# Performance work log

Measured on AMD Instinct MI355X. Metric: run time of the kernel, lower is better.

## Reference

```python
import jax, jax.numpy as jnp
import numpy as np

B, N, M, C = 4, 4096, 4096, 256
IMG_W, IMG_H = 1280.0, 384.0


def setup_inputs() -> dict:
    key = jax.random.key(0)
    ks = jax.random.split(key, 12)
    nodes_L = jax.random.normal(ks[0], (B, N, C), dtype=jnp.float32)
    nodes_R = jax.random.normal(ks[1], (B, M, C), dtype=jnp.float32)
    # pixel coordinates: (u, v) with u in [0, IMG_W), v in [0, IMG_H)
    scale = jnp.array([IMG_W, IMG_H], dtype=jnp.float32)
    kpts_L = jax.random.uniform(ks[2], (B, N, 2), dtype=jnp.float32) * scale
    kpts_R = jax.random.uniform(ks[3], (B, M, 2), dtype=jnp.float32) * scale
    s = 1.0 / np.sqrt(C)
    Wq = jax.random.normal(ks[4], (C, C), dtype=jnp.float32) * s
    bq = jnp.zeros((C,), dtype=jnp.float32)
    Wk = jax.random.normal(ks[5], (C, C), dtype=jnp.float32) * s
    bk = jnp.zeros((C,), dtype=jnp.float32)
    Wv = jax.random.normal(ks[6], (C, C), dtype=jnp.float32) * s
    bv = jnp.zeros((C,), dtype=jnp.float32)
    Wm = jax.random.normal(ks[7], (C, C), dtype=jnp.float32) * s
    bm = jnp.zeros((C,), dtype=jnp.float32)
    return {"nodes_L": nodes_L, "nodes_R": nodes_R, "kpts_L": kpts_L, "kpts_R": kpts_R,
            "Wq": Wq, "bq": bq, "Wk": Wk, "bk": bk, "Wv": Wv, "bv": bv, "Wm": Wm, "bm": bm}


def reference(nodes_L, nodes_R, kpts_L, kpts_R, Wq, bq, Wk, bk, Wv, bv, Wm, bm):
    dim = nodes_L.shape[-1]
    # torch Linear: x @ W.T + b
    Q = nodes_L @ Wq.T + bq                      # [B,N,C]
    K = nodes_R @ Wk.T + bk                      # [B,M,C]
    V = nodes_R @ Wv.T + bv                      # [B,M,C]
    # epipolar geometry terms, [B,N,M]
    dist_v = jnp.abs(kpts_L[:, :, 1:2] - kpts_R[:, :, 1][:, None, :])
    dist_u = kpts_L[:, :, 0:1] - kpts_R[:, :, 0][:, None, :]
    mask = (dist_v < 3.0) & (dist_u > 0) & (dist_u < 192)
    attn = jnp.einsum('bnc,bmc->bnm', Q, K) / jnp.sqrt(jnp.float32(dim))
    attn = jnp.where(mask, attn, jnp.float32(-1e9))
    attn_weights = jax.nn.softmax(attn, axis=-1)  # [B,N,M]
    matched = jnp.einsum('bnm,bmc->bnc', attn_weights, V)
    init_disparity = jnp.sum(attn_weights * dist_u, axis=-1, keepdims=True)  # [B,N,1]
    confidence = jnp.any(mask, axis=-1, keepdims=True).astype(jnp.float32)   # [B,N,1]
    return matched @ Wm.T + bm, init_disparity, confidence
```

## Files before the change

### kernel.cpp

```cpp
#include <hip/hip_runtime.h>
#include <hip/hip_bf16.h>

#define BB 4
#define NN 4096
#define MM 4096
#define CC 256
#define CAP 128
#define NBIN 384
#define NCH 16
#define CHK 256

typedef __attribute__((ext_vector_type(8))) short bf16x8;
typedef __attribute__((ext_vector_type(4))) float f32x4;

static __device__ __forceinline__ float bf2f(unsigned short u) {
    return __uint_as_float(((unsigned)u) << 16);
}
static __device__ __forceinline__ unsigned short f2bf(float f) {
    unsigned u = __float_as_uint(f);
    u += 0x7fffu + ((u >> 16) & 1u);
    return (unsigned short)(u >> 16);
}
static __device__ __forceinline__ bf16x8 asbf(uint4 u) {
    union { uint4 a; bf16x8 b; } c; c.a = u; return c.b;
}
static __device__ __forceinline__ void gload16(const unsigned short* g, unsigned short* l) {
    __builtin_amdgcn_global_load_lds(
        (const __attribute__((address_space(1))) unsigned int*)g,
        (__attribute__((address_space(3))) unsigned int*)l, 16, 0, 0);
}

__global__ __launch_bounds__(256) void prep_kernel(
    const float* __restrict__ Wq, const float* __restrict__ Wk,
    const float* __restrict__ Wv, const float* __restrict__ Wm,
    const float* __restrict__ L, const float* __restrict__ R,
    const float* __restrict__ kptsR,
    unsigned short* __restrict__ Wpk, unsigned short* __restrict__ Lpk,
    unsigned short* __restrict__ Rpk,
    int* __restrict__ hist, unsigned short* __restrict__ prank,
    float* __restrict__ Vsum, float* __restrict__ Usum)
{
    __shared__ __align__(16) unsigned char SMEM[32768];
    const int tid = threadIdx.x, y = blockIdx.y, x = blockIdx.x;

    if (y < 4) {
        const float* S = (y == 0) ? Wq : (y == 1) ? Wk : (y == 2) ? Wv : Wm;
        int o = x * 256 + tid;
        int j = o & 7, lane = (o >> 3) & 63, kt = o >> 9;
        int kk = kt >> 4, t = kt & 15;
        int r = t * 16 + (lane & 15), c = kk * 32 + (lane >> 4) * 8 + j;
        Wpk[(size_t)y * 65536 + o] = f2bf(S[r * 256 + c]);
        return;
    }
    if (y < 6) {
        const float* S = (y == 5) ? R : L;
        unsigned short* D = (y == 5) ? Rpk : Lpk;
        unsigned short* T = (unsigned short*)SMEM;
        const int wid = tid >> 6, lane = tid & 63;
        const size_t R0 = (size_t)x * 64;
#pragma unroll
        for (int it = 0; it < 16; ++it) {
            int row = it * 4 + wid;
            float4 f = *(const float4*)(S + (R0 + row) * 256 + lane * 4);
            ushort4 h = make_ushort4(f2bf(f.x), f2bf(f.y), f2bf(f.z), f2bf(f.w));
            int col = lane * 4;
            *(ushort4*)&T[row * 256 + (col ^ ((row & 7) << 3))] = h;
        }
        __syncthreads();
        unsigned short* Dp = D + (size_t)x * 16384;
#pragma unroll
        for (int p = 0; p < 8; ++p) {
            int u = p * 2048 + tid * 8;
            int rt = u >> 12, rem = u & 4095;
            int kk = rem >> 9, ln = (rem >> 3) & 63;
            int row = rt * 16 + (ln & 15);
            int col = kk * 32 + (ln >> 4) * 8;
            *(uint4*)(Dp + u) = *(const uint4*)&T[row * 256 + (col ^ ((row & 7) << 3))];
        }
        return;
    }
    if (y == 6) {
        if (x >= NCH * BB) return;
        int chunk = x & 15, b = x >> 4;
        int* h = (int*)SMEM;
        short* sbin = (short*)(SMEM + NBIN * 4);
        for (int i = tid; i < NBIN; i += CHK) h[i] = 0;
        int m = chunk * CHK + tid;
        float2 p = ((const float2*)kptsR)[(size_t)b * MM + m];
        int bin = (int)p.y;
        sbin[tid] = (short)bin;
        __syncthreads();
        atomicAdd(&h[bin], 1);
        int r = 0;
        for (int t = 0; t < tid; ++t) r += (sbin[t] == bin);
        prank[(b << 12) + m] = (unsigned short)r;
        __syncthreads();
        for (int i = tid; i < NBIN; i += CHK)
            hist[((size_t)b * NCH + chunk) * NBIN + i] = h[i];
        return;
    }
    if (x < BB) {
        int b = x;
        float s = 0.f;
        for (int m = tid; m < MM; m += 256) s += kptsR[((size_t)b * MM + m) * 2 + 0];
#pragma unroll
        for (int off = 32; off; off >>= 1) s += __shfl_xor(s, off);
        float* sr = (float*)SMEM;
        int wave = tid >> 6, lane = tid & 63;
        if (lane == 0) sr[wave] = s;
        __syncthreads();
        if (tid == 0) Usum[b] = sr[0] + sr[1] + sr[2] + sr[3];
    } else if (x == BB) {
        for (int i = tid; i < BB * CC; i += 256) Vsum[i] = 0.f;
    }
}

template <bool OUT_BF16>
__global__ __launch_bounds__(256, 4) void proj_mfma_kernel(
    const unsigned short* __restrict__ A0, const unsigned short* __restrict__ A1,
    const unsigned short* __restrict__ A2, const unsigned short* __restrict__ Wpk,
    const float* __restrict__ b0, const float* __restrict__ b1, const float* __restrict__ b2,
    void* __restrict__ O0, void* __restrict__ O1, void* __restrict__ O2,
    float* __restrict__ Vsum,
    const int* __restrict__ hist, int* __restrict__ binStart,
    const float* __restrict__ kptsR, const unsigned short* __restrict__ prank,
    unsigned short* __restrict__ sortedM, float2* __restrict__ sortedUV)
{
    __shared__ __align__(16) unsigned char SMEM[32768];
    const int tid = threadIdx.x, wid = tid >> 6, lane = tid & 63;
    const int y = blockIdx.y;

    if (y == 3) {
        if (blockIdx.x >= NCH * BB) return;
        const int b = blockIdx.x >> 4, chunk = blockIdx.x & 15;
        int* h2 = (int*)SMEM;
        int* sc = (int*)(SMEM + 24576);
        for (int i = tid; i < NCH * NBIN; i += 256)
            h2[i] = hist[(size_t)b * NCH * NBIN + i];
        __syncthreads();
        for (int v = tid; v < NBIN; v += 256) {
            int tot = 0;
#pragma unroll
            for (int c = 0; c < NCH; ++c) tot += h2[c * NBIN + v];
            sc[v] = tot;
        }
        __syncthreads();
        for (int off = 1; off < NBIN; off <<= 1) {
            int v1 = tid + 256;
            int t0 = (tid >= off) ? sc[tid - off] : 0;
            int t1 = (v1 < NBIN && v1 >= off) ? sc[v1 - off] : 0;
            __syncthreads();
            sc[tid] += t0;
            if (v1 < NBIN) sc[v1] += t1;
            __syncthreads();
        }
        if (chunk == 0) {
            for (int v = tid; v < NBIN; v += 256)
                binStart[b * (NBIN + 1) + v] = v ? sc[v - 1] : 0;
            if (tid == 0) binStart[b * (NBIN + 1) + NBIN] = sc[NBIN - 1];
        }
        int m = chunk * CHK + tid;
        float2 p = ((const float2*)kptsR)[(size_t)b * MM + m];
        int bin = (int)p.y;
        int ex = bin ? sc[bin - 1] : 0;
        for (int c = 0; c < chunk; ++c) ex += h2[c * NBIN + bin];
        int pos = ex + prank[(b << 12) + m];
        sortedM[(b << 12) + pos] = (unsigned short)m;
        sortedUV[(b << 12) + pos] = p;
        return;
    }

    const int lrow = lane & 15, lk = lane >> 4;
    const unsigned short* A = (y == 0) ? A0 : (y == 1) ? A1 : A2;
    const float* bias = (y == 0) ? b0 : (y == 1) ? b1 : b2;
    void* Out = (y == 0) ? O0 : (y == 1) ? O1 : O2;
    const unsigned short* W = Wpk + (size_t)y * 65536;

    const int bid = blockIdx.x;
    const int g = (bid >> 3) & 3;
    const int rblk = (bid & 7) + ((bid >> 5) << 3);
    const size_t rbase = (size_t)rblk * 128;
    const int rt0 = rblk * 8 + wid * 2;

    unsigned short* Wl = (unsigned short*)SMEM;
#pragma unroll
    for (int i = 0; i < 8; ++i) {
        int kk = wid * 2 + (i >> 2), q = i & 3;
        gload16(W + (size_t)kk * 8192 + g * 2048 + q * 512 + lane * 8,
                Wl + kk * 2048 + q * 512 + lane * 8);
    }

    const unsigned short* Ap = A + (size_t)rt0 * 4096 + lane * 8;
    uint4 a[2][2];
    a[0][0] = *(const uint4*)(Ap);
    a[0][1] = *(const uint4*)(Ap + 4096);

    f32x4 acc[4][2];
#pragma unroll
    for (int t = 0; t < 4; ++t) {
        acc[t][0] = (f32x4){0.f, 0.f, 0.f, 0.f};
        acc[t][1] = (f32x4){0.f, 0.f, 0.f, 0.f};
    }

    asm volatile("s_waitcnt vmcnt(0)" ::: "memory");
    __syncthreads();

#pragma unroll
    for (int kk = 0; kk < 8; ++kk) {
        const int cur = kk & 1, nxt = cur ^ 1;
        if (kk < 7) {
            a[nxt][0] = *(const uint4*)(Ap + (kk + 1) * 512);
            a[nxt][1] = *(const uint4*)(Ap + 4096 + (kk + 1) * 512);
        }
        bf16x8 af0 = asbf(a[cur][0]);
        bf16x8 af1 = asbf(a[cur][1]);
#pragma unroll
        for (int t = 0; t < 4; ++t) {
            bf16x8 wf = *(const bf16x8*)(Wl + kk * 2048 + t * 512 + lane * 8);
            acc[t][0] = __builtin_amdgcn_mfma_f32_16x16x32_bf16(af0, wf, acc[t][0], 0, 0, 0);
            acc[t][1] = __builtin_amdgcn_mfma_f32_16x16x32_bf16(af1, wf, acc[t][1], 0, 0, 0);
        }
    }

    if (Vsum != nullptr && y == 2) {
#pragma unroll
        for (int t = 0; t < 4; ++t) {
            int col = g * 64 + t * 16 + lrow;
            float vs = acc[t][0][0] + acc[t][0][1] + acc[t][0][2] + acc[t][0][3]
                     + acc[t][1][0] + acc[t][1][1] + acc[t][1][2] + acc[t][1][3];
            vs += __shfl_xor(vs, 16);
            vs += __shfl_xor(vs, 32);
            if (lk == 0)
                atomicAdd(&Vsum[(rblk >> 5) * CC + col], vs + 32.f * bias[col]);
        }
    }

    __syncthreads();
    if constexpr (OUT_BF16) {
        unsigned short* Bo = (unsigned short*)SMEM;
#pragma unroll
        for (int t = 0; t < 4; ++t) {
            float bb = bias[g * 64 + t * 16 + lrow];
#pragma unroll
            for (int s = 0; s < 2; ++s)
#pragma unroll
                for (int rr = 0; rr < 4; ++rr) {
                    int row = wid * 32 + s * 16 + lk * 4 + rr;
                    Bo[row * 64 + t * 16 + lrow] = f2bf(acc[t][s][rr] + bb);
                }
        }
        __syncthreads();
        unsigned short* O = (unsigned short*)Out;
#pragma unroll
        for (int it = 0; it < 4; ++it) {
            int idx = it * 2048 + tid * 8;
            int row = idx >> 6, col = idx & 63;
            *(uint4*)(O + (rbase + row) * CC + g * 64 + col) = *(const uint4*)&Bo[idx];
        }
    } else {
        float* Bo = (float*)SMEM;
#pragma unroll
        for (int t = 0; t < 4; ++t) {
            float bb = bias[g * 64 + t * 16 + lrow];
#pragma unroll
            for (int s = 0; s < 2; ++s)
#pragma unroll
                for (int rr = 0; rr < 4; ++rr) {
                    int row = wid * 32 + s * 16 + lk * 4 + rr;
                    Bo[row * 64 + t * 16 + lrow] = acc[t][s][rr] + bb;
                }
        }
        __syncthreads();
        float* O = (float*)Out;
#pragma unroll
        for (int it = 0; it < 8; ++it) {
            int idx = it * 1024 + tid * 4;
            int row = idx >> 6, col = idx & 63;
            *(float4*)(O + (rbase + row) * CC + g * 64 + col) = *(const float4*)&Bo[idx];
        }
    }
}

static __device__ __forceinline__ size_t mt_po(int bn, int lane) {
    return ((size_t)(bn >> 4)) * 4096 + (size_t)(lane >> 3) * 512
         + (size_t)(((lane >> 1) & 3) * 16 + (bn & 15)) * 8 + (lane & 1) * 4;
}

__global__ __launch_bounds__(256) void attn_kernel(
    const unsigned short* __restrict__ Q, const unsigned short* __restrict__ K,
    const unsigned short* __restrict__ V,
    const float* __restrict__ kptsL,
    const int* __restrict__ binStart, const unsigned short* __restrict__ sortedM,
    const float2* __restrict__ sortedUV,
    const float* __restrict__ Vsum, const float* __restrict__ Usum,
    unsigned short* __restrict__ Mpk, float* __restrict__ out1, float* __restrict__ out2)
{
    __shared__ unsigned short s_m[4][CAP];
    __shared__ float s_du[4][CAP];
    __shared__ float s_p[4][CAP];

    const int wid = threadIdx.x >> 6, lane = threadIdx.x & 63;
    const int bn = blockIdx.x * 4 + wid;
    const int b = bn >> 12;

    const int gi = lane >> 4, c = lane & 15;
    float qf[16];
    {
        const unsigned short* Qr = Q + (size_t)bn * CC + c * 16;
#pragma unroll
        for (int j = 0; j < 4; ++j) {
            ushort4 t = *(const ushort4*)(Qr + j * 4);
            qf[j * 4 + 0] = bf2f(t.x); qf[j * 4 + 1] = bf2f(t.y);
            qf[j * 4 + 2] = bf2f(t.z); qf[j * 4 + 3] = bf2f(t.w);
        }
    }

    float2 kl = *(const float2*)(kptsL + (size_t)bn * 2);
    float uL = kl.x, vL = kl.y;

    int ifl = (int)vL;
    int v0 = max(0, ifl - 3), v1 = min(NBIN - 1, ifl + 3);
    int s = binStart[b * (NBIN + 1) + v0];
    int e = binStart[b * (NBIN + 1) + v1 + 1];

    int cnt = 0;
    for (int i0 = s; i0 < e; i0 += 64) {
        int i = i0 + lane;
        bool valid = false;
        float du = 0.f;
        int m = 0;
        if (i < e) {
            float2 uv = sortedUV[(b << 12) + i];
            m = sortedM[(b << 12) + i];
            du = uL - uv.x;
            float dv = fabsf(vL - uv.y);
            valid = (dv < 3.0f) && (du > 0.0f) && (du < 192.0f);
        }
        unsigned long long bal = __ballot(valid);
        int pos = cnt + __popcll(bal & ((1ull << lane) - 1ull));
        if (valid && pos < CAP) { s_m[wid][pos] = (unsigned short)m; s_du[wid][pos] = du; }
        cnt += __popcll(bal);
    }
    if (cnt > CAP) cnt = CAP;

    if (cnt == 0) {
        float4 vs = *(const float4*)(Vsum + b * CC + lane * 4);
        ushort4 o = make_ushort4(f2bf(vs.x * (1.f / MM)), f2bf(vs.y * (1.f / MM)),
                                 f2bf(vs.z * (1.f / MM)), f2bf(vs.w * (1.f / MM)));
        *(ushort4*)(Mpk + mt_po(bn, lane)) = o;
        if (lane == 0) { out1[bn] = uL - Usum[b] * (1.f / MM); out2[bn] = 0.f; }
        return;
    }

    const unsigned short* Kb = K + (((size_t)b) << 12) * CC;
    for (int i0 = 0; i0 < cnt; i0 += 4) {
        int i = i0 + gi;
        int m = s_m[wid][(i < cnt) ? i : 0];
        const unsigned short* Kr = Kb + (size_t)m * CC + c * 16;
        float d = 0.f;
#pragma unroll
        for (int j = 0; j < 4; ++j) {
            ushort4 t = *(const ushort4*)(Kr + j * 4);
            d += qf[j * 4 + 0] * bf2f(t.x) + qf[j * 4 + 1] * bf2f(t.y)
               + qf[j * 4 + 2] * bf2f(t.z) + qf[j * 4 + 3] * bf2f(t.w);
        }
        d += __shfl_xor(d, 8); d += __shfl_xor(d, 4);
        d += __shfl_xor(d, 2); d += __shfl_xor(d, 1);
        if (c == 0 && i < cnt) s_p[wid][i] = d;
    }

    const float NEG = -3.0e38f;
    float mx, ps, ds, inv;
    if (cnt <= 64) {
        float x0 = (lane < cnt) ? s_p[wid][lane] * 0.0625f : NEG;
        mx = x0;
#pragma unroll
        for (int off = 32; off; off >>= 1) mx = fmaxf(mx, __shfl_xor(mx, off));
        float p0 = (lane < cnt) ? __expf(x0 - mx) : 0.f;
        float d0 = (lane < cnt) ? s_du[wid][lane] : 0.f;
        ps = p0; ds = p0 * d0;
#pragma unroll
        for (int off = 32; off; off >>= 1) { ps += __shfl_xor(ps, off); ds += __shfl_xor(ds, off); }
        inv = 1.f / ps;
        if (lane < cnt) s_p[wid][lane] = p0 * inv;
    } else {
        float x0 = (lane < cnt) ? s_p[wid][lane] * 0.0625f : NEG;
        float x1 = (lane + 64 < cnt) ? s_p[wid][lane + 64] * 0.0625f : NEG;
        mx = fmaxf(x0, x1);
#pragma unroll
        for (int off = 32; off; off >>= 1) mx = fmaxf(mx, __shfl_xor(mx, off));
        float p0 = (lane < cnt) ? __expf(x0 - mx) : 0.f;
        float p1 = (lane + 64 < cnt) ? __expf(x1 - mx) : 0.f;
        float d0 = (lane < cnt) ? s_du[wid][lane] : 0.f;
        float d1 = (lane + 64 < cnt) ? s_du[wid][lane + 64] : 0.f;
        ps = p0 + p1; ds = p0 * d0 + p1 * d1;
#pragma unroll
        for (int off = 32; off; off >>= 1) { ps += __shfl_xor(ps, off); ds += __shfl_xor(ds, off); }
        inv = 1.f / ps;
        if (lane < cnt) s_p[wid][lane] = p0 * inv;
        if (lane + 64 < cnt) s_p[wid][lane + 64] = p1 * inv;
    }

    const unsigned short* Vb = V + (((size_t)b) << 12) * CC;
    float a0 = 0.f, a1 = 0.f, a2 = 0.f, a3 = 0.f;
    float e0 = 0.f, e1 = 0.f, e2 = 0.f, e3 = 0.f;
    int i = 0;
    for (; i + 1 < cnt; i += 2) {
        float w0 = s_p[wid][i], w1 = s_p[wid][i + 1];
        ushort4 va = *(const ushort4*)(Vb + (size_t)s_m[wid][i] * CC + lane * 4);
        ushort4 vb = *(const ushort4*)(Vb + (size_t)s_m[wid][i + 1] * CC + lane * 4);
        a0 += w0 * bf2f(va.x); a1 += w0 * bf2f(va.y);
        a2 += w0 * bf2f(va.z); a3 += w0 * bf2f(va.w);
        e0 += w1 * bf2f(vb.x); e1 += w1 * bf2f(vb.y);
        e2 += w1 * bf2f(vb.z); e3 += w1 * bf2f(vb.w);
    }
    if (i < cnt) {
        float w0 = s_p[wid][i];
        ushort4 va = *(const ushort4*)(Vb + (size_t)s_m[wid][i] * CC + lane * 4);
        a0 += w0 * bf2f(va.x); a1 += w0 * bf2f(va.y);
        a2 += w0 * bf2f(va.z); a3 += w0 * bf2f(va.w);
    }
    ushort4 o = make_ushort4(f2bf(a0 + e0), f2bf(a1 + e1), f2bf(a2 + e2), f2bf(a3 + e3));
    *(ushort4*)(Mpk + mt_po(bn, lane)) = o;
    if (lane == 0) { out1[bn] = ds * inv; out2[bn] = 1.f; }
}

extern "C" void kernel_launch(void* const* d_in, const int* in_sizes, int n_in,
                              void* d_out, int out_size, void* d_ws, size_t ws_size,
                              hipStream_t stream) {
    const float* nodes_L = (const float*)d_in[0];
    const float* nodes_R = (const float*)d_in[1];
    const float* kpts_L  = (const float*)d_in[2];
    const float* kpts_R  = (const float*)d_in[3];
    const float* Wq = (const float*)d_in[4];
    const float* bq = (const float*)d_in[5];
    const float* Wk = (const float*)d_in[6];
    const float* bk = (const float*)d_in[7];
    const float* Wv = (const float*)d_in[8];
    const float* bv = (const float*)d_in[9];
    const float* Wm = (const float*)d_in[10];
    const float* bm = (const float*)d_in[11];

    char* ws = (char*)d_ws;
    unsigned short* Wpk = (unsigned short*)ws; ws += (size_t)4 * 65536 * 2;
    unsigned short* Lpk = (unsigned short*)ws; ws += (size_t)BB * NN * CC * 2;
    unsigned short* Rpk = (unsigned short*)ws; ws += (size_t)BB * MM * CC * 2;
    unsigned short* Qp  = (unsigned short*)ws; ws += (size_t)BB * NN * CC * 2;
    unsigned short* Kp  = (unsigned short*)ws; ws += (size_t)BB * MM * CC * 2;
    unsigned short* Vp  = (unsigned short*)ws; ws += (size_t)BB * MM * CC * 2;
    unsigned short* Mpk = (unsigned short*)ws; ws += (size_t)BB * NN * CC * 2;
    float* Vsum = (float*)ws;        ws += (size_t)BB * CC * 4;
    float* Usum = (float*)ws;        ws += (size_t)BB * 4;
    float2* sortedUV = (float2*)ws;  ws += (size_t)BB * MM * 8;
    int* binStart = (int*)ws;        ws += (size_t)BB * (NBIN + 1) * 4;
    unsigned short* sortedM = (unsigned short*)ws; ws += (size_t)BB * MM * 2;
    int* hist = (int*)ws;            ws += (size_t)BB * NCH * NBIN * 4;
    unsigned short* prank = (unsigned short*)ws;

    float* out0 = (float*)d_out;
    float* out1 = out0 + (size_t)BB * NN * CC;
    float* out2 = out1 + (size_t)BB * NN;

    prep_kernel<<<dim3(256, 8), dim3(256), 0, stream>>>(
        Wq, Wk, Wv, Wm, nodes_L, nodes_R, kpts_R,
        Wpk, Lpk, Rpk, hist, prank, Vsum, Usum);

    proj_mfma_kernel<true><<<dim3(512, 4), dim3(256), 0, stream>>>(
        Lpk, Rpk, Rpk, Wpk, bq, bk, bv, Qp, Kp, Vp, Vsum,
        hist, binStart, kpts_R, prank, sortedM, sortedUV);

    attn_kernel<<<dim3(BB * NN / 4), dim3(256), 0, stream>>>(
        Qp, Kp, Vp, kpts_L, binStart, sortedM, sortedUV, Vsum, Usum, Mpk, out1, out2);

    proj_mfma_kernel<false><<<dim3(512, 1), dim3(256), 0, stream>>>(
        Mpk, nullptr, nullptr, Wpk + 3 * 65536, bm, nullptr, nullptr,
        out0, nullptr, nullptr, nullptr,
        nullptr, nullptr, nullptr, nullptr, nullptr, nullptr);
}
```

Before: 62.77 us.

## Process left keypoints in v-bin sorted order for K/V locality in attention

```diff
diff --git a/kernel.cpp b/kernel.cpp
--- a/kernel.cpp
+++ b/kernel.cpp
@@ -34,10 +34,11 @@
     const float* __restrict__ Wq, const float* __restrict__ Wk,
     const float* __restrict__ Wv, const float* __restrict__ Wm,
     const float* __restrict__ L, const float* __restrict__ R,
-    const float* __restrict__ kptsR,
+    const float* __restrict__ kptsR, const float* __restrict__ kptsL,
     unsigned short* __restrict__ Wpk, unsigned short* __restrict__ Lpk,
     unsigned short* __restrict__ Rpk,
     int* __restrict__ hist, unsigned short* __restrict__ prank,
+    int* __restrict__ histL, unsigned short* __restrict__ prankL,
     float* __restrict__ Vsum, float* __restrict__ Usum)
 {
     __shared__ __align__(16) unsigned char SMEM[32768];
@@ -79,24 +80,27 @@
         }
         return;
     }
-    if (y == 6) {
+    if (y == 6 || y == 8) {
         if (x >= NCH * BB) return;
+        const float* KP = (y == 8) ? kptsL : kptsR;
+        int* H = (y == 8) ? histL : hist;
+        unsigned short* PR = (y == 8) ? prankL : prank;
         int chunk = x & 15, b = x >> 4;
         int* h = (int*)SMEM;
         short* sbin = (short*)(SMEM + NBIN * 4);
         for (int i = tid; i < NBIN; i += CHK) h[i] = 0;
         int m = chunk * CHK + tid;
-        float2 p = ((const float2*)kptsR)[(size_t)b * MM + m];
+        float2 p = ((const float2*)KP)[(size_t)b * MM + m];
         int bin = (int)p.y;
         sbin[tid] = (short)bin;
         __syncthreads();
         atomicAdd(&h[bin], 1);
         int r = 0;
         for (int t = 0; t < tid; ++t) r += (sbin[t] == bin);
-        prank[(b << 12) + m] = (unsigned short)r;
+        PR[(b << 12) + m] = (unsigned short)r;
         __syncthreads();
         for (int i = tid; i < NBIN; i += CHK)
-            hist[((size_t)b * NCH + chunk) * NBIN + i] = h[i];
+            H[((size_t)b * NCH + chunk) * NBIN + i] = h[i];
         return;
     }
     if (x < BB) {
@@ -122,21 +126,27 @@
     const float* __restrict__ b0, const float* __restrict__ b1, const float* __restrict__ b2,
     void* __restrict__ O0, void* __restrict__ O1, void* __restrict__ O2,
     float* __restrict__ Vsum,
-    const int* __restrict__ hist, int* __restrict__ binStart,
-    const float* __restrict__ kptsR, const unsigned short* __restrict__ prank,
-    unsigned short* __restrict__ sortedM, float2* __restrict__ sortedUV)
+    const int* __restrict__ hist, const int* __restrict__ histL,
+    int* __restrict__ binStart,
+    const float* __restrict__ kptsR, const float* __restrict__ kptsL,
+    const unsigned short* __restrict__ prank, const unsigned short* __restrict__ prankL,
+    unsigned short* __restrict__ sortedM, float2* __restrict__ sortedUV,
+    unsigned short* __restrict__ sortedNL)
 {
     __shared__ __align__(16) unsigned char SMEM[32768];
     const int tid = threadIdx.x, wid = tid >> 6, lane = tid & 63;
     const int y = blockIdx.y;
 
     if (y == 3) {
-        if (blockIdx.x >= NCH * BB) return;
-        const int b = blockIdx.x >> 4, chunk = blockIdx.x & 15;
+        if (blockIdx.x >= 2 * NCH * BB) return;
+        const int isL = blockIdx.x >= NCH * BB;
+        const int xx = blockIdx.x & (NCH * BB - 1);
+        const int b = xx >> 4, chunk = xx & 15;
+        const int* H = isL ? histL : hist;
         int* h2 = (int*)SMEM;
         int* sc = (int*)(SMEM + 24576);
         for (int i = tid; i < NCH * NBIN; i += 256)
-            h2[i] = hist[(size_t)b * NCH * NBIN + i];
+            h2[i] = H[(size_t)b * NCH * NBIN + i];
         __syncthreads();
         for (int v = tid; v < NBIN; v += 256) {
             int tot = 0;
@@ -154,19 +164,23 @@
             if (v1 < NBIN) sc[v1] += t1;
             __syncthreads();
         }
-        if (chunk == 0) {
+        if (!isL && chunk == 0) {
             for (int v = tid; v < NBIN; v += 256)
                 binStart[b * (NBIN + 1) + v] = v ? sc[v - 1] : 0;
             if (tid == 0) binStart[b * (NBIN + 1) + NBIN] = sc[NBIN - 1];
         }
         int m = chunk * CHK + tid;
-        float2 p = ((const float2*)kptsR)[(size_t)b * MM + m];
+        float2 p = ((const float2*)(isL ? kptsL : kptsR))[(size_t)b * MM + m];
         int bin = (int)p.y;
         int ex = bin ? sc[bin - 1] : 0;
         for (int c = 0; c < chunk; ++c) ex += h2[c * NBIN + bin];
-        int pos = ex + prank[(b << 12) + m];
-        sortedM[(b << 12) + pos] = (unsigned short)m;
-        sortedUV[(b << 12) + pos] = p;
+        int pos = ex + (isL ? prankL : prank)[(b << 12) + m];
+        if (isL) {
+            sortedNL[(b << 12) + pos] = (unsigned short)m;
+        } else {
+            sortedM[(b << 12) + pos] = (unsigned short)m;
+            sortedUV[(b << 12) + pos] = p;
+        }
         return;
     }
 
@@ -289,7 +303,7 @@
 __global__ __launch_bounds__(256) void attn_kernel(
     const unsigned short* __restrict__ Q, const unsigned short* __restrict__ K,
     const unsigned short* __restrict__ V,
-    const float* __restrict__ kptsL,
+    const float* __restrict__ kptsL, const unsigned short* __restrict__ sortedNL,
     const int* __restrict__ binStart, const unsigned short* __restrict__ sortedM,
     const float2* __restrict__ sortedUV,
     const float* __restrict__ Vsum, const float* __restrict__ Usum,
@@ -300,8 +314,10 @@
     __shared__ float s_p[4][CAP];
 
     const int wid = threadIdx.x >> 6, lane = threadIdx.x & 63;
-    const int bn = blockIdx.x * 4 + wid;
-    const int b = bn >> 12;
+    const int bid = (blockIdx.x & 7) * 512 + (blockIdx.x >> 3);
+    const int si = bid * 4 + wid;
+    const int b = si >> 12;
+    const int bn = (b << 12) + sortedNL[si];
 
     const int gi = lane >> 4, c = lane & 15;
     float qf[16];
@@ -455,25 +471,31 @@
     int* binStart = (int*)ws;        ws += (size_t)BB * (NBIN + 1) * 4;
     unsigned short* sortedM = (unsigned short*)ws; ws += (size_t)BB * MM * 2;
     int* hist = (int*)ws;            ws += (size_t)BB * NCH * NBIN * 4;
-    unsigned short* prank = (unsigned short*)ws;
+    unsigned short* prank = (unsigned short*)ws;   ws += (size_t)BB * MM * 2;
+    int* histL = (int*)ws;           ws += (size_t)BB * NCH * NBIN * 4;
+    unsigned short* prankL = (unsigned short*)ws;  ws += (size_t)BB * NN * 2;
+    unsigned short* sortedNL = (unsigned short*)ws;
 
     float* out0 = (float*)d_out;
     float* out1 = out0 + (size_t)BB * NN * CC;
     float* out2 = out1 + (size_t)BB * NN;
 
-    prep_kernel<<<dim3(256, 8), dim3(256), 0, stream>>>(
-        Wq, Wk, Wv, Wm, nodes_L, nodes_R, kpts_R,
-        Wpk, Lpk, Rpk, hist, prank, Vsum, Usum);
+    prep_kernel<<<dim3(256, 9), dim3(256), 0, stream>>>(
+        Wq, Wk, Wv, Wm, nodes_L, nodes_R, kpts_R, kpts_L,
+        Wpk, Lpk, Rpk, hist, prank, histL, prankL, Vsum, Usum);
 
     proj_mfma_kernel<true><<<dim3(512, 4), dim3(256), 0, stream>>>(
         Lpk, Rpk, Rpk, Wpk, bq, bk, bv, Qp, Kp, Vp, Vsum,
-        hist, binStart, kpts_R, prank, sortedM, sortedUV);
+        hist, histL, binStart, kpts_R, kpts_L, prank, prankL,
+        sortedM, sortedUV, sortedNL);
 
     attn_kernel<<<dim3(BB * NN / 4), dim3(256), 0, stream>>>(
-        Qp, Kp, Vp, kpts_L, binStart, sortedM, sortedUV, Vsum, Usum, Mpk, out1, out2);
+        Qp, Kp, Vp, kpts_L, sortedNL, binStart, sortedM, sortedUV,
+        Vsum, Usum, Mpk, out1, out2);
 
     proj_mfma_kernel<false><<<dim3(512, 1), dim3(256), 0, stream>>>(
         Mpk, nullptr, nullptr, Wpk + 3 * 65536, bm, nullptr, nullptr,
         out0, nullptr, nullptr, nullptr,
-        nullptr, nullptr, nullptr, nullptr, nullptr, nullptr);
-}
+        nullptr, nullptr, nullptr, nullptr, nullptr, nullptr, nullptr,
+        nullptr, nullptr, nullptr);
+}
```

Measured after the change: 60.53 us. -3.6%, faster.
